# Performance work log

Hardware: AMD Instinct MI355X
Metric: run time of the kernel (lower is better)

Reference implementation:

```python
import jax, jax.numpy as jnp
import numpy as np


def _conv3d(x, w, stride, pad):
    return jax.lax.conv_general_dilated(
        x, w, window_strides=stride, padding=[(p, p) for p in pad],
        dimension_numbers=('NCDHW', 'OIDHW', 'NCDHW'))


def _bn(x, g, b, eps=1e-5):
    # BatchNorm3d in training mode: batch statistics over (N, D, H, W)
    m = x.mean((0, 2, 3, 4), keepdims=True)
    v = ((x - m) ** 2).mean((0, 2, 3, 4), keepdims=True)
    return (x - m) * jax.lax.rsqrt(v + eps) * g.reshape(1, -1, 1, 1, 1) + b.reshape(1, -1, 1, 1, 1)


def _lrelu(x):
    return jnp.where(x >= 0, x, 0.2 * x)


def _deform_conv3d(x, off, w, stride, pad, n_off_groups):
    # Deformable conv3d: offsets predict per-output-location (dz,dy,dx) shifts for
    # every kernel tap, shared across channel groups of size C//n_off_groups.
    B, C, D, H, W = x.shape
    O, _, kd, kh, kw = w.shape
    K = kd * kh * kw
    sd, sh, sw = stride
    pd, ph, pw = pad
    Do = (D + 2 * pd - kd) // sd + 1
    Ho = (H + 2 * ph - kh) // sh + 1
    Wo = (W + 2 * pw - kw) // sw + 1
    G = n_off_groups
    Cg = C // G
    # offset layout: [B, G, K, 3(dz,dy,dx), Do, Ho, Wo]
    off = off.reshape(B, G, K, 3, Do, Ho, Wo)
    kz, ky, kx = jnp.meshgrid(jnp.arange(kd), jnp.arange(kh), jnp.arange(kw), indexing='ij')
    bz = (jnp.arange(Do) * sd - pd).astype(x.dtype)[:, None, None]
    by = (jnp.arange(Ho) * sh - ph).astype(x.dtype)[None, :, None]
    bx = (jnp.arange(Wo) * sw - pw).astype(x.dtype)[None, None, :]
    kb = lambda a: a.reshape(-1).astype(x.dtype)[None, None, :, None, None, None]
    pz = off[:, :, :, 0] + bz + kb(kz)   # [B,G,K,Do,Ho,Wo]
    py = off[:, :, :, 1] + by + kb(ky)
    px = off[:, :, :, 2] + bx + kb(kx)
    z0, y0, x0 = jnp.floor(pz), jnp.floor(py), jnp.floor(px)
    fz, fy, fx = pz - z0, py - y0, px - x0
    xg = x.reshape(B, G, Cg, D * H * W)
    acc = jnp.zeros((B, G, Cg, K, Do, Ho, Wo), x.dtype)
    for cz in (0, 1):
        for cy in (0, 1):
            for cx in (0, 1):
                zc, yc, xc = z0 + cz, y0 + cy, x0 + cx
                wgt = ((fz if cz else 1 - fz) * (fy if cy else 1 - fy) * (fx if cx else 1 - fx))
                valid = ((zc >= 0) & (zc <= D - 1) & (yc >= 0) & (yc <= H - 1)
                         & (xc >= 0) & (xc <= W - 1)).astype(x.dtype)
                zi = jnp.clip(zc, 0, D - 1).astype(jnp.int32)
                yi = jnp.clip(yc, 0, H - 1).astype(jnp.int32)
                xi = jnp.clip(xc, 0, W - 1).astype(jnp.int32)
                idx = ((zi * H + yi) * W + xi).reshape(B, G, 1, -1)
                v = jnp.take_along_axis(xg, jnp.broadcast_to(idx, (B, G, Cg, idx.shape[-1])), axis=3)
                acc = acc + (wgt * valid)[:, :, None] * v.reshape(B, G, Cg, K, Do, Ho, Wo)
    val = acc.reshape(B, C, K, Do, Ho, Wo)
    return jnp.einsum('bckdhw,ock->bodhw', val, w.reshape(O, C, K))


def setup_inputs() -> dict:
    key = jax.random.key(0)
    ks = jax.random.split(key, 24)
    f32 = jnp.float32
    p = lambda k, shape, s=0.05: jax.random.normal(k, shape, f32) * s
    gb = lambda k, c: (1.0 + 0.05 * jax.random.normal(k, (c,), f32),
                       0.05 * jax.random.normal(jax.random.fold_in(k, 1), (c,), f32))
    g2, b2 = gb(ks[8], 64)
    g3, b3 = gb(ks[9], 128)
    g4, b4 = gb(ks[10], 256)
    g5, b5 = gb(ks[11], 512)
    g6, b6 = gb(ks[12], 512)
    return {
        'input': jax.random.normal(ks[0], (64, 3, 8, 128, 128), f32),
        'w1': p(ks[1], (32, 3, 4, 4, 4)),
        'w2': p(ks[2], (64, 32, 2, 4, 4)),
        'w3': p(ks[3], (128, 64, 2, 4, 4)),
        'w4': p(ks[4], (256, 128, 1, 4, 4)),
        'w_off': p(ks[5], (192, 256, 1, 4, 4), 0.01),
        'w5': p(ks[6], (512, 256, 1, 4, 4)),
        'w6': p(ks[7], (512, 512, 1, 4, 4)),
        'g2': g2, 'b2': b2, 'g3': g3, 'b3': b3, 'g4': g4, 'b4': b4,
        'g5': g5, 'b5': b5, 'g6': g6, 'b6': b6,
    }


def reference(input, w1, w2, w3, w4, w_off, w5, w6,
              g2, b2, g3, b3, g4, b4, g5, b5, g6, b6):
    encs = []
    out = _lrelu(_conv3d(input, w1, (2, 2, 2), (1, 1, 1)))          # norm_1 unused in forward
    encs.append(out)
    out = _lrelu(_bn(_conv3d(out, w2, (1, 2, 2), (0, 1, 1)), g2, b2))
    encs.append(out)
    out = _lrelu(_bn(_conv3d(out, w3, (1, 2, 2), (0, 1, 1)), g3, b3))
    encs.append(out)
    out = _lrelu(_bn(_conv3d(out, w4, (1, 2, 2), (0, 1, 1)), g4, b4))
    encs.append(out)
    off = _conv3d(out, w_off, (1, 2, 2), (0, 1, 1))
    out = _lrelu(_bn(_deform_conv3d(out, off, w5, (1, 2, 2), (0, 1, 1), 4), g5, b5))
    encs.append(out)
    out = _lrelu(_bn(_conv3d(out, w6, (1, 1, 1), (0, 0, 0)), g6, b6))
    encs.append(out)
    return tuple(encs)
```

## Files before the change

kernel.cpp:

```cpp
#include <hip/hip_runtime.h>
#include <hip/hip_bf16.h>
#include <cstdint>

typedef short bf16x8 __attribute__((ext_vector_type(8)));
typedef float f32x4 __attribute__((ext_vector_type(4)));

__device__ __forceinline__ float lrelu_f(float y) { return y >= 0.f ? y : 0.2f * y; }
__device__ __forceinline__ float b2f(unsigned short u) {
    union { unsigned int i; float f; } v; v.i = ((unsigned int)u) << 16; return v.f;
}
__device__ __forceinline__ unsigned short f2b(float f) {
    union { unsigned int i; float f; } v; v.f = f;
    unsigned int r = v.i + 0x7FFFu + ((v.i >> 16) & 1u);
    return (unsigned short)(r >> 16);
}

__global__ __launch_bounds__(256) void xin_cl_k(const float* __restrict__ x,
                                                unsigned short* __restrict__ xc)
{
    int i = blockIdx.x * 256 + threadIdx.x;
    int c = i & 3, w = (i >> 2) & 127, h = (i >> 9) & 127, d = (i >> 16) & 7, b = i >> 19;
    float v = (c < 3) ? x[(((size_t)b * 3 + c) * 8 + d) * 16384 + h * 128 + w] : 0.f;
    xc[i] = f2b(v);
}

__global__ __launch_bounds__(256) void repack_all(
    const float* __restrict__ w1, const float* __restrict__ w2,
    const float* __restrict__ w3, const float* __restrict__ w4,
    const float* __restrict__ w_off, const float* __restrict__ w5,
    const float* __restrict__ w6, unsigned short* __restrict__ wp)
{
    long i = (long)blockIdx.x * 256 + threadIdx.x;
    const float* src; int Cin, Tap, Cip; long rel;
    if (i < 8192)         { src = w1;    Cin = 3;   Tap = 64; Cip = 4;   rel = i; }
    else if (i < 73728)   { src = w2;    Cin = 32;  Tap = 32; Cip = 32;  rel = i - 8192; }
    else if (i < 335872)  { src = w3;    Cin = 64;  Tap = 32; Cip = 64;  rel = i - 73728; }
    else if (i < 860160)  { src = w4;    Cin = 128; Tap = 16; Cip = 128; rel = i - 335872; }
    else if (i < 1646592) { src = w_off; Cin = 256; Tap = 16; Cip = 256; rel = i - 860160; }
    else if (i < 3743744) { src = w5;    Cin = 256; Tap = 16; Cip = 256; rel = i - 1646592; }
    else                  { src = w6;    Cin = 512; Tap = 16; Cip = 512; rel = i - 3743744; }
    int c = (int)(rel % Cip);
    long t1 = rel / Cip;
    int t = (int)(t1 % Tap);
    long o = t1 / Tap;
    wp[i] = (c < Cin) ? f2b(src[((size_t)o * Cin + c) * Tap + t]) : (unsigned short)0;
}

template<int BN, int AMODE, int EPI>
__global__ __launch_bounds__(256) void igemm(
    const unsigned short* __restrict__ A, const unsigned short* __restrict__ Bw,
    void* __restrict__ Cout, float* __restrict__ sums,
    int M, int N, int K, int klen,
    int Ci, int Di, int Hi, int Wi,
    int kd, int kh, int kw,
    int sd, int sh_, int sw_, int pd, int ph_, int pw_,
    int Do, int Ho, int Wo)
{
    constexpr int NF = BN / 32;
    constexpr int WN = 16 * NF;
    constexpr int NBU = (BN * 4 + 255) / 256;
    constexpr int NAU = (AMODE == 2) ? 4 : 2;
    constexpr int ASTR = 4 * 128 * 8;
    constexpr int BSTR = 4 * BN * 8;
    __shared__ __align__(16) unsigned short As[2][4][128][8];
    __shared__ __align__(16) unsigned short Bs[2][4][BN][8];
    __shared__ float redbuf[(EPI == 4) ? 2 * BN : 1];
    const int tid = threadIdx.x;
    const int m0 = blockIdx.x * 128;
    const int n0 = blockIdx.y * BN;
    const int k0 = blockIdx.z * klen;
    const int kend = min(K, k0 + klen);
    unsigned short* const As0 = &As[0][0][0][0];
    unsigned short* const Bs0 = &Bs[0][0][0][0];

    size_t bsrc[NBU];
    int boff[NBU];
#pragma unroll
    for (int i = 0; i < NBU; ++i) {
        int u = tid + i * 256;
        int row = u >> 2, s = u & 3;
        if (BN * 4 >= 256 || u < BN * 4) {
            bsrc[i] = (size_t)(n0 + row) * K + s * 8;
            boff[i] = (s * BN + row) * 8;
        }
    }

    size_t asz[2];
    int asrc[NAU];
    unsigned long long amask[NAU];
    int aoff[NAU];

    if constexpr (AMODE == 0) {
#pragma unroll
        for (int i = 0; i < 2; ++i) {
            int u = tid + i * 256;
            int r = u >> 2, s = u & 3;
            asz[i] = (size_t)(m0 + r) * K + s * 8;
            aoff[i] = (s * 128 + r) * 8;
        }
    } else {
#pragma unroll
        for (int i = 0; i < NAU; ++i) {
            int u = tid + i * 256;
            int r = (AMODE == 2) ? (u >> 3) : (u >> 2);
            int m = m0 + r;
            int ow = m % Wo; int t1 = m / Wo;
            int oh = t1 % Ho; t1 /= Ho;
            int od = t1 % Do; int b = t1 / Do;
            int id0 = od * sd - pd, ih0 = oh * sh_ - ph_, iw0 = ow * sw_ - pw_;
            unsigned long long xm = 0ull, yx = 0ull, mask = 0ull;
            for (int p = 0; p < kw; ++p) if ((unsigned)(iw0 + p) < (unsigned)Wi) xm |= 1ull << p;
            for (int p = 0; p < kh; ++p) if ((unsigned)(ih0 + p) < (unsigned)Hi) yx |= xm << (p * kw);
            for (int p = 0; p < kd; ++p) if ((unsigned)(id0 + p) < (unsigned)Di) mask |= yx << (p * kh * kw);
            amask[i] = mask;
            int bsp = ((b * Di + id0) * Hi + ih0) * Wi + iw0;
            if constexpr (AMODE == 1) {
                int s = u & 3;
                asrc[i] = bsp * Ci + s * 8;
                aoff[i] = (s * 128 + r) * 8;
            } else {
                int j = u & 7;
                asrc[i] = (bsp + (j >> 2) * Wi + (j & 3)) * 4;
                aoff[i] = ((j >> 1) * 128 + r) * 8 + (j & 1) * 4;
            }
        }
    }

    f32x4 acc[4][NF];
#pragma unroll
    for (int i = 0; i < 4; ++i)
#pragma unroll
        for (int j = 0; j < NF; ++j) acc[i][j] = (f32x4){0.f, 0.f, 0.f, 0.f};

    const int lane = tid & 63, wv = tid >> 6;
    const int wm = wv >> 1, wn = wv & 1;
    const int kg = lane >> 4, fr = lane & 15;

    int c0 = 0, kx = 0, ky = 0, tap = 0, doff = 0;
    if constexpr (AMODE == 1) {
        c0 = k0 % Ci;
        tap = k0 / Ci;
        kx = tap % kw;
        int t2 = tap / kw;
        ky = t2 % kh;
        int kz = t2 / kh;
        doff = (kz * Hi + ky) * Wi + kx;
    }
    auto advance = [&]() {
        c0 += 32;
        if (c0 >= Ci) {
            c0 = 0; ++tap; ++kx; ++doff;
            if (kx == kw) {
                kx = 0; doff += Wi - kw; ++ky;
                if (ky == kh) { ky = 0; doff += (Hi - kh) * Wi; }
            }
        }
    };

    for (int k = k0; k < kend; k += 64) {
#pragma unroll
        for (int i = 0; i < NBU; ++i)
            if (BN * 4 >= 256 || tid + i * 256 < BN * 4) {
                uint4 v0 = *(const uint4*)&Bw[bsrc[i] + k];
                uint4 v1 = *(const uint4*)&Bw[bsrc[i] + k + 32];
                *(uint4*)(Bs0 + boff[i]) = v0;
                *(uint4*)(Bs0 + BSTR + boff[i]) = v1;
            }
        if constexpr (AMODE == 0) {
#pragma unroll
            for (int i = 0; i < 2; ++i) {
                uint4 v0 = *(const uint4*)&A[asz[i] + k];
                uint4 v1 = *(const uint4*)&A[asz[i] + k + 32];
                *(uint4*)(As0 + aoff[i]) = v0;
                *(uint4*)(As0 + ASTR + aoff[i]) = v1;
            }
        } else if constexpr (AMODE == 1) {
            int t0 = tap, d0 = doff * Ci + c0;
            advance();
            int t1 = tap, d1 = doff * Ci + c0;
            advance();
#pragma unroll
            for (int i = 0; i < 2; ++i) {
                uint4 v0 = {0u, 0u, 0u, 0u}, v1 = {0u, 0u, 0u, 0u};
                if ((amask[i] >> t0) & 1ull) v0 = *(const uint4*)&A[(size_t)(asrc[i] + d0)];
                if ((amask[i] >> t1) & 1ull) v1 = *(const uint4*)&A[(size_t)(asrc[i] + d1)];
                *(uint4*)(As0 + aoff[i]) = v0;
                *(uint4*)(As0 + ASTR + aoff[i]) = v1;
            }
        } else {
            int kz = k >> 6;
            int U0 = kz * (Hi * Wi) * 4;
            int U1 = U0 + 2 * Wi * 4;
            int tap0 = k >> 2;
#pragma unroll
            for (int i = 0; i < 4; ++i) {
                int j = (tid + i * 256) & 7;
                uint2 v0 = {0u, 0u}, v1 = {0u, 0u};
                if ((amask[i] >> (tap0 + j)) & 1ull)
                    v0 = *(const uint2*)&A[(size_t)(asrc[i] + U0)];
                if ((amask[i] >> (tap0 + 8 + j)) & 1ull)
                    v1 = *(const uint2*)&A[(size_t)(asrc[i] + U1)];
                *(uint2*)(As0 + aoff[i]) = v0;
                *(uint2*)(As0 + ASTR + aoff[i]) = v1;
            }
        }
        __syncthreads();
#pragma unroll
        for (int kb = 0; kb < 2; ++kb) {
            bf16x8 af[4], bfr[NF];
#pragma unroll
            for (int mi = 0; mi < 4; ++mi)
                af[mi] = *(const bf16x8*)&As[kb][kg][wm * 64 + mi * 16 + fr][0];
#pragma unroll
            for (int ni = 0; ni < NF; ++ni)
                bfr[ni] = *(const bf16x8*)&Bs[kb][kg][wn * WN + ni * 16 + fr][0];
#pragma unroll
            for (int mi = 0; mi < 4; ++mi)
#pragma unroll
                for (int ni = 0; ni < NF; ++ni)
                    acc[mi][ni] = __builtin_amdgcn_mfma_f32_16x16x32_bf16(af[mi], bfr[ni], acc[mi][ni], 0, 0, 0);
        }
        __syncthreads();
    }

    if constexpr (EPI == 4) {
        for (int j = tid; j < 2 * BN; j += 256) redbuf[j] = 0.f;
        __syncthreads();
    }
    const int rb = m0 + wm * 64 + (lane >> 4) * 4;
    const int cb = n0 + wn * WN + fr;
    float p1[NF], p2[NF];
    if constexpr (EPI == 4) {
#pragma unroll
        for (int ni = 0; ni < NF; ++ni) { p1[ni] = 0.f; p2[ni] = 0.f; }
    }
#pragma unroll
    for (int mi = 0; mi < 4; ++mi)
#pragma unroll
        for (int rg = 0; rg < 4; ++rg) {
            size_t rowbase = (size_t)(rb + mi * 16 + rg) * N;
#pragma unroll
            for (int ni = 0; ni < NF; ++ni) {
                size_t idx = rowbase + cb + ni * 16;
                float vv = acc[mi][ni][rg];
                if constexpr (EPI == 0) ((unsigned short*)Cout)[idx] = f2b(vv);
                else if constexpr (EPI == 1) ((float*)Cout)[idx] = vv;
                else if constexpr (EPI == 2) atomicAdd((float*)Cout + idx, vv);
                else if constexpr (EPI == 3) ((unsigned short*)Cout)[idx] = f2b(lrelu_f(vv));
                else {
                    ((unsigned short*)Cout)[idx] = f2b(vv);
                    p1[ni] += vv; p2[ni] += vv * vv;
                }
            }
        }
    if constexpr (EPI == 4) {
#pragma unroll
        for (int ni = 0; ni < NF; ++ni) {
            int cl = wn * WN + ni * 16 + fr;
            atomicAdd(&redbuf[cl], p1[ni]);
            atomicAdd(&redbuf[BN + cl], p2[ni]);
        }
        __syncthreads();
        for (int j = tid; j < 2 * BN; j += 256) {
            int gcol = (j < BN) ? (n0 + j) : (N + n0 + j - BN);
            atomicAdd(&sums[gcol], redbuf[j]);
        }
    }
}

__global__ __launch_bounds__(256) void f2b_sums(const float* __restrict__ in,
                                                unsigned short* __restrict__ o,
                                                float* __restrict__ sums,
                                                long totalSlots, int C)
{
    const int tid = threadIdx.x;
    long gid = (long)blockIdx.x * 256 + tid;
    long stride = (long)gridDim.x * 256;
    float s1[8], s2[8];
#pragma unroll
    for (int j = 0; j < 8; ++j) { s1[j] = 0.f; s2[j] = 0.f; }
    for (long s = gid; s < totalSlots; s += stride) {
        float4 a = *(const float4*)&in[s * 8];
        float4 b = *(const float4*)&in[s * 8 + 4];
        float f[8] = {a.x, a.y, a.z, a.w, b.x, b.y, b.z, b.w};
        unsigned short u[8];
#pragma unroll
        for (int j = 0; j < 8; ++j) { u[j] = f2b(f[j]); s1[j] += f[j]; s2[j] += f[j] * f[j]; }
        *(uint4*)&o[s * 8] = *(uint4*)u;
    }
    __shared__ float r1[2048], r2[2048];
#pragma unroll
    for (int j = 0; j < 8; ++j) { r1[tid * 8 + j] = s1[j]; r2[tid * 8 + j] = s2[j]; }
    __syncthreads();
    int G = C >> 3;
    for (int c = tid; c < C; c += 256) {
        int grp = c >> 3, j = c & 7;
        float a = 0.f, b = 0.f;
        for (int th = grp; th < 256; th += G) { a += r1[th * 8 + j]; b += r2[th * 8 + j]; }
        atomicAdd(&sums[c], a);
        atomicAdd(&sums[C + c], b);
    }
}

__global__ __launch_bounds__(256) void bn_fin(float* __restrict__ sums,
                                              const float* __restrict__ g, const float* __restrict__ bt,
                                              float* __restrict__ sc, float* __restrict__ sh,
                                              int C, float invcnt)
{
    int c = blockIdx.x * 256 + threadIdx.x;
    if (c >= C) return;
    float mean = sums[c] * invcnt;
    float var = sums[C + c] * invcnt - mean * mean;
    float rs = rsqrtf(var + 1e-5f);
    float scl = g[c] * rs;
    sc[c] = scl;
    sh[c] = bt[c] - mean * scl;
    sums[c] = 0.f;
    sums[C + c] = 0.f;
}

template<int MODE>
__global__ __launch_bounds__(256) void bn_apply_t(
    unsigned short* __restrict__ x, const float* __restrict__ sc, const float* __restrict__ sh,
    float* __restrict__ outN, int C, int TC, int S)
{
    __shared__ __align__(16) float T[64][68];
    const int tid = threadIdx.x;
    const long m0 = (long)blockIdx.x * 64;
    const int c0 = blockIdx.y * TC;
    const int spr = TC >> 3;
    const int lg = (spr == 8) ? 3 : 2;
    const int tot = 64 * spr;
    for (int u = tid; u < tot; u += 256) {
        int r = u >> lg, sl = u & (spr - 1);
        size_t idx = (size_t)(m0 + r) * C + c0 + sl * 8;
        uint4 v = *(uint4*)&x[idx];
        unsigned short* pv = (unsigned short*)&v;
#pragma unroll
        for (int j = 0; j < 8; ++j) {
            int c = c0 + sl * 8 + j;
            float f = b2f(pv[j]);
            if (MODE == 1) {
                f = lrelu_f(f * sc[c] + sh[c]);
                pv[j] = f2b(f);
            }
            T[sl * 8 + j][r] = f;
        }
        if (MODE == 1) *(uint4*)&x[idx] = v;
    }
    __syncthreads();
    const int tpc = 256 / TC;
    const int rpt = 64 / tpc;
    int cl = tid / tpc;
    int r0 = (tid % tpc) * rpt;
    int c = c0 + cl;
    if ((S & 63) == 0) {
        long b = m0 / S;
        long s0 = m0 - b * S;
        float* op = outN + ((size_t)b * C + c) * S + s0 + r0;
        for (int r = 0; r < rpt; r += 4)
            *(float4*)(op + r) = *(float4*)&T[cl][r0 + r];
    } else {
        for (int r = 0; r < rpt; ++r) {
            long m = m0 + r0 + r;
            long b = m / S, s = m - b * S;
            outN[((size_t)b * C + c) * S + s] = T[cl][r0 + r];
        }
    }
}

__global__ __launch_bounds__(256) void deform_val(
    const unsigned short* __restrict__ xcl, const float* __restrict__ offc,
    unsigned short* __restrict__ val)
{
    int bs = blockIdx.x;
    int b = bs >> 5, s = bs & 31;
    int od = s >> 4, oh = (s >> 2) & 3, ow = s & 3;
    __shared__ float cw[64][8];
    __shared__ int cidx[64][8];
    int tid = threadIdx.x;
    if (tid < 64) {
        int gk = tid, k = gk & 15;
        int ky = k >> 2, kx = k & 3;
        const float* op = offc + (size_t)bs * 192 + gk * 3;
        float pz = op[0] + (float)od;
        float py = op[1] + (float)(oh * 2 - 1 + ky);
        float px = op[2] + (float)(ow * 2 - 1 + kx);
        float z0 = floorf(pz), y0 = floorf(py), x0 = floorf(px);
        float fz = pz - z0, fy = py - y0, fx = px - x0;
#pragma unroll
        for (int ci = 0; ci < 8; ++ci) {
            int cz = ci >> 2, cy = (ci >> 1) & 1, cx = ci & 1;
            float zc = z0 + cz, yc = y0 + cy, xc = x0 + cx;
            bool ok = zc >= 0.f && zc <= 1.f && yc >= 0.f && yc <= 7.f && xc >= 0.f && xc <= 7.f;
            int zi = min(max((int)zc, 0), 1);
            int yi = min(max((int)yc, 0), 7);
            int xi = min(max((int)xc, 0), 7);
            float wz = cz ? fz : 1.f - fz;
            float wy = cy ? fy : 1.f - fy;
            float wx = cx ? fx : 1.f - fx;
            cw[gk][ci] = ok ? wz * wy * wx : 0.f;
            cidx[gk][ci] = (zi * 8 + yi) * 8 + xi;
        }
    }
    __syncthreads();
    const unsigned short* xb = xcl + (size_t)b * 128 * 256;
    unsigned short* vo = val + (size_t)bs * 4096;
    for (int j = tid; j < 4096; j += 256) {
        int c = j & 255, tap = j >> 8;
        int gk = ((c >> 6) << 4) | tap;
        float v = 0.f;
#pragma unroll
        for (int i = 0; i < 8; ++i)
            v += cw[gk][i] * b2f(xb[(size_t)cidx[gk][i] * 256 + c]);
        vo[j] = f2b(v);
    }
}

extern "C" void kernel_launch(void* const* d_in, const int* in_sizes, int n_in,
                              void* d_out, int out_size, void* d_ws, size_t ws_size,
                              hipStream_t stream)
{
    (void)in_sizes; (void)n_in; (void)out_size; (void)ws_size;
    const float* x     = (const float*)d_in[0];
    const float* w1    = (const float*)d_in[1];
    const float* w2    = (const float*)d_in[2];
    const float* w3    = (const float*)d_in[3];
    const float* w4    = (const float*)d_in[4];
    const float* w_off = (const float*)d_in[5];
    const float* w5    = (const float*)d_in[6];
    const float* w6    = (const float*)d_in[7];
    const float* g2 = (const float*)d_in[8];  const float* b2 = (const float*)d_in[9];
    const float* g3 = (const float*)d_in[10]; const float* b3 = (const float*)d_in[11];
    const float* g4 = (const float*)d_in[12]; const float* b4 = (const float*)d_in[13];
    const float* g5 = (const float*)d_in[14]; const float* b5 = (const float*)d_in[15];
    const float* g6 = (const float*)d_in[16]; const float* b6 = (const float*)d_in[17];

    float* out = (float*)d_out;
    float* enc0 = out;
    float* enc1 = out + 33554432;
    float* enc2 = out + 46137344;
    float* enc3 = out + 50331648;
    float* enc4 = out + 52428800;
    float* enc5 = out + 53477376;

    char* W = (char*)d_ws;
    unsigned short* wpk  = (unsigned short*)(W + 0);
    unsigned short* w1p  = (unsigned short*)(W + 0);
    unsigned short* w2p  = (unsigned short*)(W + 16384);
    unsigned short* w3p  = (unsigned short*)(W + 147456);
    unsigned short* w4p  = (unsigned short*)(W + 671744);
    unsigned short* wofp = (unsigned short*)(W + 1720320);
    unsigned short* w5p  = (unsigned short*)(W + 3293184);
    unsigned short* w6p  = (unsigned short*)(W + 7487488);
    float* sums          = (float*)(W + 15876096);
    float* sc            = (float*)(W + 15880192);
    float* sh            = (float*)(W + 15882240);
    float* offc          = (float*)(W + 15884288);
    unsigned short* xcl  = (unsigned short*)(W + 17457152);
    unsigned short* e1c  = (unsigned short*)(W + 17457152);
    unsigned short* e2c  = (unsigned short*)(W + 42622976);
    unsigned short* e3c  = (unsigned short*)(W + 51011584);
    unsigned short* e0c  = (unsigned short*)(W + 84566016);
    unsigned short* valb = (unsigned short*)(W + 84566016);
    float* raw5          = (float*)(W + 101343232);
    unsigned short* e4c  = (unsigned short*)(W + 105537536);
    float* raw6          = (float*)(W + 107634688);
    unsigned short* e5c  = (unsigned short*)(W + 107896832);

    hipMemsetAsync(sums, 0, 4096, stream);
    xin_cl_k<<<131072, 256, 0, stream>>>(x, xcl);
    repack_all<<<31008, 256, 0, stream>>>(w1, w2, w3, w4, w_off, w5, w6, wpk);

    igemm<32, 2, 3><<<dim3(8192, 1, 1), 256, 0, stream>>>(
        xcl, w1p, e0c, nullptr, 1048576, 32, 256, 256,
        4, 8, 128, 128, 4, 4, 4, 2, 2, 2, 1, 1, 1, 4, 64, 64);
    bn_apply_t<0><<<dim3(16384, 1), 256, 0, stream>>>(e0c, nullptr, nullptr, enc0, 32, 32, 16384);

    igemm<64, 1, 4><<<dim3(1536, 1, 1), 256, 0, stream>>>(
        e0c, w2p, e1c, sums, 196608, 64, 1024, 1024,
        32, 4, 64, 64, 2, 4, 4, 1, 2, 2, 0, 1, 1, 3, 32, 32);
    bn_fin<<<1, 256, 0, stream>>>(sums, g2, b2, sc, sh, 64, 1.f / 196608.f);
    bn_apply_t<1><<<dim3(3072, 1), 256, 0, stream>>>(e1c, sc, sh, enc1, 64, 64, 3072);

    igemm<128, 1, 4><<<dim3(256, 1, 1), 256, 0, stream>>>(
        e1c, w3p, e2c, sums, 32768, 128, 2048, 2048,
        64, 3, 32, 32, 2, 4, 4, 1, 2, 2, 0, 1, 1, 2, 16, 16);
    bn_fin<<<1, 256, 0, stream>>>(sums, g3, b3, sc, sh, 128, 1.f / 32768.f);
    bn_apply_t<1><<<dim3(512, 2), 256, 0, stream>>>(e2c, sc, sh, enc2, 128, 64, 512);

    igemm<64, 1, 4><<<dim3(64, 4), 256, 0, stream>>>(
        e2c, w4p, e3c, sums, 8192, 256, 2048, 2048,
        128, 2, 16, 16, 1, 4, 4, 1, 2, 2, 0, 1, 1, 2, 8, 8);
    bn_fin<<<1, 256, 0, stream>>>(sums, g4, b4, sc, sh, 256, 1.f / 8192.f);
    bn_apply_t<1><<<dim3(128, 4), 256, 0, stream>>>(e3c, sc, sh, enc3, 256, 64, 128);

    hipMemsetAsync(offc, 0, 1572864, stream);
    igemm<64, 1, 2><<<dim3(16, 3, 8), 256, 0, stream>>>(
        e3c, wofp, offc, nullptr, 2048, 192, 4096, 512,
        256, 2, 8, 8, 1, 4, 4, 1, 2, 2, 0, 1, 1, 2, 4, 4);

    deform_val<<<2048, 256, 0, stream>>>(e3c, offc, valb);
    hipMemsetAsync(raw5, 0, 4194304, stream);
    igemm<64, 0, 2><<<dim3(16, 8, 8), 256, 0, stream>>>(
        valb, w5p, raw5, nullptr, 2048, 512, 4096, 512,
        0, 0, 0, 0, 1, 1, 1, 1, 1, 1, 0, 0, 0, 1, 1, 1);
    f2b_sums<<<256, 256, 0, stream>>>(raw5, e4c, sums, 131072L, 512);
    bn_fin<<<2, 256, 0, stream>>>(sums, g5, b5, sc, sh, 512, 1.f / 2048.f);
    bn_apply_t<1><<<dim3(32, 8), 256, 0, stream>>>(e4c, sc, sh, enc4, 512, 64, 32);

    hipMemsetAsync(raw6, 0, 262144, stream);
    igemm<64, 0, 2><<<dim3(1, 8, 32), 256, 0, stream>>>(
        e4c, w6p, raw6, nullptr, 128, 512, 8192, 256,
        0, 0, 0, 0, 1, 1, 1, 1, 1, 1, 0, 0, 0, 1, 1, 1);
    f2b_sums<<<32, 256, 0, stream>>>(raw6, e5c, sums, 8192L, 512);
    bn_fin<<<2, 256, 0, stream>>>(sums, g6, b6, sc, sh, 512, 1.f / 128.f);
    bn_apply_t<1><<<dim3(2, 8), 256, 0, stream>>>(e5c, sc, sh, enc5, 512, 64, 2);
}
```

Baseline: 586.4 us.

## Template igemm on M-tile size and fuse layer-1 NCDHW output write into GEMM epilogue

Makes the GEMM M-tile (and so the thread count) a template parameter. The first conv and the two large BN convs now use 256-row tiles with 512 threads. A new epilogue mode writes the layer-1 activation straight to the fp32 NCDHW output as float4 stores, which removes the separate bn_apply_t<0> transpose pass. Larger tiles reuse the weight tile more and halve the block count, at the cost of more LDS and registers per block and fewer blocks.

```diff
diff --git a/kernel.cpp b/kernel.cpp
--- a/kernel.cpp
+++ b/kernel.cpp
@@ -46,8 +46,8 @@
     wp[i] = (c < Cin) ? f2b(src[((size_t)o * Cin + c) * Tap + t]) : (unsigned short)0;
 }
 
-template<int BN, int AMODE, int EPI>
-__global__ __launch_bounds__(256) void igemm(
+template<int TM, int BN, int AMODE, int EPI>
+__global__ __launch_bounds__(TM * 2) void igemm(
     const unsigned short* __restrict__ A, const unsigned short* __restrict__ Bw,
     void* __restrict__ Cout, float* __restrict__ sums,
     int M, int N, int K, int klen,
@@ -56,17 +56,18 @@
     int sd, int sh_, int sw_, int pd, int ph_, int pw_,
     int Do, int Ho, int Wo)
 {
+    constexpr int NT = TM * 2;
     constexpr int NF = BN / 32;
     constexpr int WN = 16 * NF;
-    constexpr int NBU = (BN * 4 + 255) / 256;
+    constexpr int NBU = (BN * 4 + NT - 1) / NT;
     constexpr int NAU = (AMODE == 2) ? 4 : 2;
-    constexpr int ASTR = 4 * 128 * 8;
+    constexpr int ASTR = 4 * TM * 8;
     constexpr int BSTR = 4 * BN * 8;
-    __shared__ __align__(16) unsigned short As[2][4][128][8];
+    __shared__ __align__(16) unsigned short As[2][4][TM][8];
     __shared__ __align__(16) unsigned short Bs[2][4][BN][8];
     __shared__ float redbuf[(EPI == 4) ? 2 * BN : 1];
     const int tid = threadIdx.x;
-    const int m0 = blockIdx.x * 128;
+    const int m0 = blockIdx.x * TM;
     const int n0 = blockIdx.y * BN;
     const int k0 = blockIdx.z * klen;
     const int kend = min(K, k0 + klen);
@@ -77,9 +78,9 @@
     int boff[NBU];
 #pragma unroll
     for (int i = 0; i < NBU; ++i) {
-        int u = tid + i * 256;
+        int u = tid + i * NT;
         int row = u >> 2, s = u & 3;
-        if (BN * 4 >= 256 || u < BN * 4) {
+        if (BN * 4 >= NT || u < BN * 4) {
             bsrc[i] = (size_t)(n0 + row) * K + s * 8;
             boff[i] = (s * BN + row) * 8;
         }
@@ -93,15 +94,15 @@
     if constexpr (AMODE == 0) {
 #pragma unroll
         for (int i = 0; i < 2; ++i) {
-            int u = tid + i * 256;
+            int u = tid + i * NT;
             int r = u >> 2, s = u & 3;
             asz[i] = (size_t)(m0 + r) * K + s * 8;
-            aoff[i] = (s * 128 + r) * 8;
+            aoff[i] = (s * TM + r) * 8;
         }
     } else {
 #pragma unroll
         for (int i = 0; i < NAU; ++i) {
-            int u = tid + i * 256;
+            int u = tid + i * NT;
             int r = (AMODE == 2) ? (u >> 3) : (u >> 2);
             int m = m0 + r;
             int ow = m % Wo; int t1 = m / Wo;
@@ -117,11 +118,11 @@
             if constexpr (AMODE == 1) {
                 int s = u & 3;
                 asrc[i] = bsp * Ci + s * 8;
-                aoff[i] = (s * 128 + r) * 8;
+                aoff[i] = (s * TM + r) * 8;
             } else {
                 int j = u & 7;
                 asrc[i] = (bsp + (j >> 2) * Wi + (j & 3)) * 4;
-                aoff[i] = ((j >> 1) * 128 + r) * 8 + (j & 1) * 4;
+                aoff[i] = ((j >> 1) * TM + r) * 8 + (j & 1) * 4;
             }
         }
     }
@@ -160,7 +161,7 @@
     for (int k = k0; k < kend; k += 64) {
 #pragma unroll
         for (int i = 0; i < NBU; ++i)
-            if (BN * 4 >= 256 || tid + i * 256 < BN * 4) {
+            if (BN * 4 >= NT || tid + i * NT < BN * 4) {
                 uint4 v0 = *(const uint4*)&Bw[bsrc[i] + k];
                 uint4 v1 = *(const uint4*)&Bw[bsrc[i] + k + 32];
                 *(uint4*)(Bs0 + boff[i]) = v0;
@@ -194,7 +195,7 @@
             int tap0 = k >> 2;
 #pragma unroll
             for (int i = 0; i < 4; ++i) {
-                int j = (tid + i * 256) & 7;
+                int j = (tid + i * NT) & 7;
                 uint2 v0 = {0u, 0u}, v1 = {0u, 0u};
                 if ((amask[i] >> (tap0 + j)) & 1ull)
                     v0 = *(const uint2*)&A[(size_t)(asrc[i] + U0)];
@@ -224,7 +225,7 @@
     }
 
     if constexpr (EPI == 4) {
-        for (int j = tid; j < 2 * BN; j += 256) redbuf[j] = 0.f;
+        for (int j = tid; j < 2 * BN; j += NT) redbuf[j] = 0.f;
         __syncthreads();
     }
     const int rb = m0 + wm * 64 + (lane >> 4) * 4;
@@ -246,7 +247,7 @@
                 if constexpr (EPI == 0) ((unsigned short*)Cout)[idx] = f2b(vv);
                 else if constexpr (EPI == 1) ((float*)Cout)[idx] = vv;
                 else if constexpr (EPI == 2) atomicAdd((float*)Cout + idx, vv);
-                else if constexpr (EPI == 3) ((unsigned short*)Cout)[idx] = f2b(lrelu_f(vv));
+                else if constexpr (EPI == 3 || EPI == 5) ((unsigned short*)Cout)[idx] = f2b(lrelu_f(vv));
                 else {
                     ((unsigned short*)Cout)[idx] = f2b(vv);
                     p1[ni] += vv; p2[ni] += vv * vv;
@@ -261,9 +262,22 @@
             atomicAdd(&redbuf[BN + cl], p2[ni]);
         }
         __syncthreads();
-        for (int j = tid; j < 2 * BN; j += 256) {
+        for (int j = tid; j < 2 * BN; j += NT) {
             int gcol = (j < BN) ? (n0 + j) : (N + n0 + j - BN);
             atomicAdd(&sums[gcol], redbuf[j]);
+        }
+    }
+    if constexpr (EPI == 5) {
+#pragma unroll
+        for (int mi = 0; mi < 4; ++mi) {
+            int mr = rb + mi * 16;
+            int b = mr >> 14, ssp = mr & 16383;
+            float4 f;
+            f.x = lrelu_f(acc[mi][0][0]);
+            f.y = lrelu_f(acc[mi][0][1]);
+            f.z = lrelu_f(acc[mi][0][2]);
+            f.w = lrelu_f(acc[mi][0][3]);
+            *(float4*)&sums[((size_t)(b * 32 + cb)) * 16384 + ssp] = f;
         }
     }
 }
@@ -319,7 +333,6 @@
     sums[C + c] = 0.f;
 }
 
-template<int MODE>
 __global__ __launch_bounds__(256) void bn_apply_t(
     unsigned short* __restrict__ x, const float* __restrict__ sc, const float* __restrict__ sh,
     float* __restrict__ outN, int C, int TC, int S)
@@ -340,13 +353,11 @@
         for (int j = 0; j < 8; ++j) {
             int c = c0 + sl * 8 + j;
             float f = b2f(pv[j]);
-            if (MODE == 1) {
-                f = lrelu_f(f * sc[c] + sh[c]);
-                pv[j] = f2b(f);
-            }
+            f = lrelu_f(f * sc[c] + sh[c]);
+            pv[j] = f2b(f);
             T[sl * 8 + j][r] = f;
         }
-        if (MODE == 1) *(uint4*)&x[idx] = v;
+        *(uint4*)&x[idx] = v;
     }
     __syncthreads();
     const int tpc = 256 / TC;
@@ -472,48 +483,47 @@
     xin_cl_k<<<131072, 256, 0, stream>>>(x, xcl);
     repack_all<<<31008, 256, 0, stream>>>(w1, w2, w3, w4, w_off, w5, w6, wpk);
 
-    igemm<32, 2, 3><<<dim3(8192, 1, 1), 256, 0, stream>>>(
-        xcl, w1p, e0c, nullptr, 1048576, 32, 256, 256,
+    igemm<256, 32, 2, 5><<<dim3(4096, 1, 1), 512, 0, stream>>>(
+        xcl, w1p, e0c, enc0, 1048576, 32, 256, 256,
         4, 8, 128, 128, 4, 4, 4, 2, 2, 2, 1, 1, 1, 4, 64, 64);
-    bn_apply_t<0><<<dim3(16384, 1), 256, 0, stream>>>(e0c, nullptr, nullptr, enc0, 32, 32, 16384);
-
-    igemm<64, 1, 4><<<dim3(1536, 1, 1), 256, 0, stream>>>(
+
+    igemm<256, 64, 1, 4><<<dim3(768, 1, 1), 512, 0, stream>>>(
         e0c, w2p, e1c, sums, 196608, 64, 1024, 1024,
         32, 4, 64, 64, 2, 4, 4, 1, 2, 2, 0, 1, 1, 3, 32, 32);
     bn_fin<<<1, 256, 0, stream>>>(sums, g2, b2, sc, sh, 64, 1.f / 196608.f);
-    bn_apply_t<1><<<dim3(3072, 1), 256, 0, stream>>>(e1c, sc, sh, enc1, 64, 64, 3072);
-
-    igemm<128, 1, 4><<<dim3(256, 1, 1), 256, 0, stream>>>(
+    bn_apply_t<<<dim3(3072, 1), 256, 0, stream>>>(e1c, sc, sh, enc1, 64, 64, 3072);
+
+    igemm<256, 64, 1, 4><<<dim3(128, 2), 512, 0, stream>>>(
         e1c, w3p, e2c, sums, 32768, 128, 2048, 2048,
         64, 3, 32, 32, 2, 4, 4, 1, 2, 2, 0, 1, 1, 2, 16, 16);
     bn_fin<<<1, 256, 0, stream>>>(sums, g3, b3, sc, sh, 128, 1.f / 32768.f);
-    bn_apply_t<1><<<dim3(512, 2), 256, 0, stream>>>(e2c, sc, sh, enc2, 128, 64, 512);
-
-    igemm<64, 1, 4><<<dim3(64, 4), 256, 0, stream>>>(
+    bn_apply_t<<<dim3(512, 2), 256, 0, stream>>>(e2c, sc, sh, enc2, 128, 64, 512);
+
+    igemm<128, 64, 1, 4><<<dim3(64, 4), 256, 0, stream>>>(
         e2c, w4p, e3c, sums, 8192, 256, 2048, 2048,
         128, 2, 16, 16, 1, 4, 4, 1, 2, 2, 0, 1, 1, 2, 8, 8);
     bn_fin<<<1, 256, 0, stream>>>(sums, g4, b4, sc, sh, 256, 1.f / 8192.f);
-    bn_apply_t<1><<<dim3(128, 4), 256, 0, stream>>>(e3c, sc, sh, enc3, 256, 64, 128);
+    bn_apply_t<<<dim3(128, 4), 256, 0, stream>>>(e3c, sc, sh, enc3, 256, 64, 128);
 
     hipMemsetAsync(offc, 0, 1572864, stream);
-    igemm<64, 1, 2><<<dim3(16, 3, 8), 256, 0, stream>>>(
+    igemm<128, 64, 1, 2><<<dim3(16, 3, 8), 256, 0, stream>>>(
         e3c, wofp, offc, nullptr, 2048, 192, 4096, 512,
         256, 2, 8, 8, 1, 4, 4, 1, 2, 2, 0, 1, 1, 2, 4, 4);
 
     deform_val<<<2048, 256, 0, stream>>>(e3c, offc, valb);
     hipMemsetAsync(raw5, 0, 4194304, stream);
-    igemm<64, 0, 2><<<dim3(16, 8, 8), 256, 0, stream>>>(
+    igemm<128, 64, 0, 2><<<dim3(16, 8, 8), 256, 0, stream>>>(
         valb, w5p, raw5, nullptr, 2048, 512, 4096, 512,
         0, 0, 0, 0, 1, 1, 1, 1, 1, 1, 0, 0, 0, 1, 1, 1);
     f2b_sums<<<256, 256, 0, stream>>>(raw5, e4c, sums, 131072L, 512);
     bn_fin<<<2, 256, 0, stream>>>(sums, g5, b5, sc, sh, 512, 1.f / 2048.f);
-    bn_apply_t<1><<<dim3(32, 8), 256, 0, stream>>>(e4c, sc, sh, enc4, 512, 64, 32);
+    bn_apply_t<<<dim3(32, 8), 256, 0, stream>>>(e4c, sc, sh, enc4, 512, 64, 32);
 
     hipMemsetAsync(raw6, 0, 262144, stream);
-    igemm<64, 0, 2><<<dim3(1, 8, 32), 256, 0, stream>>>(
+    igemm<128, 64, 0, 2><<<dim3(1, 8, 32), 256, 0, stream>>>(
         e4c, w6p, raw6, nullptr, 128, 512, 8192, 256,
         0, 0, 0, 0, 1, 1, 1, 1, 1, 1, 0, 0, 0, 1, 1, 1);
     f2b_sums<<<32, 256, 0, stream>>>(raw6, e5c, sums, 8192L, 512);
     bn_fin<<<2, 256, 0, stream>>>(sums, g6, b6, sc, sh, 512, 1.f / 128.f);
-    bn_apply_t<1><<<dim3(2, 8), 256, 0, stream>>>(e5c, sc, sh, enc5, 512, 64, 2);
-}
+    bn_apply_t<<<dim3(2, 8), 256, 0, stream>>>(e5c, sc, sh, enc5, 512, 64, 2);
+}
```

New measurement: 553.4 us. 1.06x faster.
